# Performance work log

Hardware: AMD Instinct MI355X
Metric: run time of the kernel (lower is better)

## Reference

```python
import jax, jax.numpy as jnp
import numpy as np

B, N, D, M, H = 16, 196, 512, 20, 8


def setup_inputs() -> dict:
    key = jax.random.key(0)
    ks = jax.random.split(key, 8)
    s = 0.02  # small init scale for stable activations
    return {
        "F_clean": jax.random.normal(ks[0], (B, N, D), dtype=jnp.float32),
        "in_proj_w": jax.random.normal(ks[1], (3 * D, D), dtype=jnp.float32) * s,
        "in_proj_b": jnp.zeros((3 * D,), jnp.float32),
        "out_w": jax.random.normal(ks[2], (D, D), dtype=jnp.float32) * s,
        "out_b": jnp.zeros((D,), jnp.float32),
        "w1": jax.random.normal(ks[3], (D, D), dtype=jnp.float32) * s,
        "b1": jnp.zeros((D,), jnp.float32),
        "ln_g": jnp.ones((D,), jnp.float32),
        "ln_b": jnp.zeros((D,), jnp.float32),
        "w2": jax.random.normal(ks[4], (M, D), dtype=jnp.float32) * s,
        "b2": jnp.zeros((M,), jnp.float32),
        "templates": jax.random.normal(ks[5], (M, D), dtype=jnp.float32),
        "k": 51,  # int(D * sparsity_ratio=0.1)
    }


def reference(F_clean, in_proj_w, in_proj_b, out_w, out_b, w1, b1, ln_g, ln_b, w2, b2, templates, k):
    b, n, d = F_clean.shape
    hd = d // H
    # --- MultiheadAttention (batch_first, dropout inactive at eval) ---
    qkv = F_clean @ in_proj_w.T + in_proj_b  # [B,N,3D]
    q, kk, v = jnp.split(qkv, 3, axis=-1)
    to_heads = lambda x: x.reshape(b, n, H, hd).transpose(0, 2, 1, 3)  # [B,H,N,hd]
    q, kk, v = to_heads(q), to_heads(kk), to_heads(v)
    attn = jax.nn.softmax(jnp.einsum('bhqd,bhkd->bhqk', q, kk) / jnp.sqrt(jnp.float32(hd)), axis=-1)
    o = jnp.einsum('bhqk,bhkd->bhqd', attn, v).transpose(0, 2, 1, 3).reshape(b, n, d)
    F_enh = o @ out_w.T + out_b + F_clean  # residual
    # --- decompose MLP: Linear -> LayerNorm -> GELU(exact) -> Linear ---
    h = F_enh @ w1.T + b1
    mu = h.mean(-1, keepdims=True)
    var = h.var(-1, keepdims=True)
    h = (h - mu) / jnp.sqrt(var + 1e-5) * ln_g + ln_b
    h = jax.nn.gelu(h, approximate=False)
    Qp = h @ w2.T + b2  # [B,N,M]
    # --- outer-product expansion: [B,N,D,M] ---
    Q = F_clean[:, :, :, None] * templates.T[None, None] * Qp[:, :, None, :]
    # --- per-(b,n,m) abs-topk over D, scatter 0/1 mask, L2-normalize over D ---
    A = Q.transpose(0, 1, 3, 2)  # [B,N,M,D]
    _, idx = jax.lax.top_k(jnp.abs(A), k)
    mask = jnp.put_along_axis(jnp.zeros(A.shape, A.dtype), idx, 1.0, axis=-1, inplace=False)
    Qs = A * mask
    nrm = jnp.sqrt(jnp.sum(Qs * Qs, axis=-1, keepdims=True))
    Qn = Qs / jnp.maximum(nrm, 1e-6)  # torch F.normalize clamps norm to eps
    return Qn.transpose(0, 1, 3, 2)  # [B,N,D,M]
```

## Files before the change

kernel.cpp:

```cpp
#include <hip/hip_runtime.h>
#include <cmath>


typedef __attribute__((ext_vector_type(8))) short bf16x8v;
typedef __attribute__((ext_vector_type(4))) float f32x4v;

__device__ __forceinline__ unsigned short f2bf_rne(float x) {
  unsigned u = __float_as_uint(x);
  u += 0x7fffu + ((u >> 16) & 1u);
  return (unsigned short)(u >> 16);
}
__device__ __forceinline__ float bf2f(unsigned short h) {
  return __uint_as_float(((unsigned)h) << 16);
}
__device__ __forceinline__ void split3_1(float x,
    unsigned short& s0, unsigned short& s1, unsigned short& s2) {
  s0 = f2bf_rne(x); float r1 = x - bf2f(s0);
  s1 = f2bf_rne(r1); float r2 = r1 - bf2f(s1);
  s2 = f2bf_rne(r2);
}
__device__ __forceinline__ void split3_8(const float* xs,
    bf16x8v& o0, bf16x8v& o1, bf16x8v& o2) {
#pragma unroll
  for (int e = 0; e < 8; e++) {
    unsigned short a, b, c;
    split3_1(xs[e], a, b, c);
    o0[e] = (short)a; o1[e] = (short)b; o2[e] = (short)c;
  }
}

__global__ __launch_bounds__(256) void split4_kernel(
    const float* __restrict__ X0, unsigned short* __restrict__ O0, int n0,
    const float* __restrict__ X1, unsigned short* __restrict__ O1, int n1,
    const float* __restrict__ X2, unsigned short* __restrict__ O2, int n2,
    const float* __restrict__ X3, unsigned short* __restrict__ O3, int n3)
{
  int nb0 = n0 >> 11, nb1 = n1 >> 11, nb2 = n2 >> 11;
  int b = blockIdx.x;
  const float* X; unsigned short* O; long long i8, n;
  if (b < nb0)                   { X = X0; O = O0; n = n0; i8 = (long long)b * 256 + threadIdx.x; }
  else if (b < nb0 + nb1)        { X = X1; O = O1; n = n1; i8 = (long long)(b - nb0) * 256 + threadIdx.x; }
  else if (b < nb0 + nb1 + nb2)  { X = X2; O = O2; n = n2; i8 = (long long)(b - nb0 - nb1) * 256 + threadIdx.x; }
  else                           { X = X3; O = O3; n = n3; i8 = (long long)(b - nb0 - nb1 - nb2) * 256 + threadIdx.x; }
  const float4 aa = *(const float4*)(X + i8 * 8);
  const float4 bb = *(const float4*)(X + i8 * 8 + 4);
  float xs[8] = {aa.x, aa.y, aa.z, aa.w, bb.x, bb.y, bb.z, bb.w};
  bf16x8v o0, o1, o2;
  split3_8(xs, o0, o1, o2);
  *(bf16x8v*)(O + i8 * 8)          = o0;
  *(bf16x8v*)(O + n + i8 * 8)      = o1;
  *(bf16x8v*)(O + 2 * n + i8 * 8)  = o2;
}

#define GBK 32
#define AROWB 80
#define SPLIT_SZ (128 * AROWB)
#define BBASE (3 * SPLIT_SZ)

__global__ __launch_bounds__(256) void gemm_ps3_kernel(
    const unsigned short* __restrict__ As, const unsigned short* __restrict__ Bs,
    float* __restrict__ C, const float* __restrict__ bias,
    const float* __restrict__ res,
    int M, int N, int ldc, long long aPlane, long long bPlane,
    unsigned short* __restrict__ Cl, long long clPlane)
{
  __shared__ __align__(16) unsigned char smem[2 * BBASE];

  int tid = threadIdx.x;
  int lane = tid & 63, w = tid >> 6;
  int wrow = w >> 1, wcol = w & 1;
  int i0 = blockIdx.x * 128, j0 = blockIdx.y * 128;

  int r = tid >> 1, hh = tid & 1;
  int arow = i0 + r; if (arow > M - 1) arow = M - 1;
  int brow = j0 + r; if (brow > N - 1) brow = N - 1;
  const unsigned short* ap = As + (size_t)arow * 512 + hh * 16;
  const unsigned short* bp = Bs + (size_t)brow * 512 + hh * 16;
  unsigned swoff = (unsigned)r * AROWB + (unsigned)hh * 32;

  f32x4v acc[4][4];
#pragma unroll
  for (int fi = 0; fi < 4; fi++)
#pragma unroll
    for (int fj = 0; fj < 4; fj++) acc[fi][fj] = (f32x4v){0.f, 0.f, 0.f, 0.f};

  unsigned fr_a = (unsigned)(wrow * 64 + (lane & 15)) * AROWB + (unsigned)(lane >> 4) * 16;
  unsigned fr_b = (unsigned)(wcol * 64 + (lane & 15)) * AROWB + (unsigned)(lane >> 4) * 16 + BBASE;

  for (int k0 = 0; k0 < 512; k0 += GBK) {
    bf16x8v a0[3], a1[3], b0v[3], b1v[3];
#pragma unroll
    for (int s = 0; s < 3; s++) {
      a0[s]  = *(const bf16x8v*)(ap + s * aPlane + k0);
      a1[s]  = *(const bf16x8v*)(ap + s * aPlane + k0 + 8);
      b0v[s] = *(const bf16x8v*)(bp + s * bPlane + k0);
      b1v[s] = *(const bf16x8v*)(bp + s * bPlane + k0 + 8);
    }
    __syncthreads();
#pragma unroll
    for (int s = 0; s < 3; s++) {
      *(bf16x8v*)(smem + s * SPLIT_SZ + swoff)              = a0[s];
      *(bf16x8v*)(smem + s * SPLIT_SZ + swoff + 16)         = a1[s];
      *(bf16x8v*)(smem + BBASE + s * SPLIT_SZ + swoff)      = b0v[s];
      *(bf16x8v*)(smem + BBASE + s * SPLIT_SZ + swoff + 16) = b1v[s];
    }
    __syncthreads();

    bf16x8v af[4][3];
#pragma unroll
    for (int fi = 0; fi < 4; fi++)
#pragma unroll
      for (int s = 0; s < 3; s++)
        af[fi][s] = *(const bf16x8v*)(smem + s * SPLIT_SZ + fr_a + fi * (16 * AROWB));

#pragma unroll
    for (int fj = 0; fj < 4; fj++) {
      bf16x8v b0 = *(const bf16x8v*)(smem + 0 * SPLIT_SZ + fr_b + fj * (16 * AROWB));
      bf16x8v b1 = *(const bf16x8v*)(smem + 1 * SPLIT_SZ + fr_b + fj * (16 * AROWB));
      bf16x8v b2 = *(const bf16x8v*)(smem + 2 * SPLIT_SZ + fr_b + fj * (16 * AROWB));
#pragma unroll
      for (int fi = 0; fi < 4; fi++) {
        f32x4v c = acc[fi][fj];
        c = __builtin_amdgcn_mfma_f32_16x16x32_bf16(af[fi][2], b0, c, 0, 0, 0);
        c = __builtin_amdgcn_mfma_f32_16x16x32_bf16(af[fi][1], b1, c, 0, 0, 0);
        c = __builtin_amdgcn_mfma_f32_16x16x32_bf16(af[fi][0], b2, c, 0, 0, 0);
        c = __builtin_amdgcn_mfma_f32_16x16x32_bf16(af[fi][1], b0, c, 0, 0, 0);
        c = __builtin_amdgcn_mfma_f32_16x16x32_bf16(af[fi][0], b1, c, 0, 0, 0);
        c = __builtin_amdgcn_mfma_f32_16x16x32_bf16(af[fi][0], b0, c, 0, 0, 0);
        acc[fi][fj] = c;
      }
    }
  }

#pragma unroll
  for (int fi = 0; fi < 4; fi++) {
    int row0 = i0 + wrow * 64 + fi * 16 + (lane >> 4) * 4;
#pragma unroll
    for (int fj = 0; fj < 4; fj++) {
      int col = j0 + wcol * 64 + fj * 16 + (lane & 15);
      if (col >= N) continue;
      float badd = bias ? bias[col] : 0.0f;
      f32x4v v = acc[fi][fj];
#pragma unroll
      for (int rr = 0; rr < 4; rr++) {
        int row = row0 + rr;
        if (row < M) {
          float o = v[rr] + badd;
          if (res) o += res[(size_t)row * ldc + col];
          size_t idx = (size_t)row * ldc + col;
          if (Cl) {
            unsigned short l0, l1, l2;
            split3_1(o, l0, l1, l2);
            Cl[idx] = l0; Cl[idx + clPlane] = l1; Cl[idx + 2 * clPlane] = l2;
          } else {
            C[idx] = o;
          }
        }
      }
    }
  }
}

__global__ __launch_bounds__(256) void gemm_bf16x3_kernel(
    const float* __restrict__ A, const float* __restrict__ B,
    float* __restrict__ C, const float* __restrict__ bias,
    const float* __restrict__ res,
    int M, int N, int K, int lda, int ldb, int ldc,
    int zInner, long long aOuter, long long aInner,
    long long bOuter, long long bInner,
    long long cOuter, long long cInner,
    unsigned short* __restrict__ Cl, long long clPlane)
{
  int z = blockIdx.z;
  int zo = z / zInner, zi = z % zInner;
  A += zo * aOuter + zi * aInner;
  B += zo * bOuter + zi * bInner;
  long long coff = zo * cOuter + zi * cInner;
  if (C) C += coff;
  if (Cl) Cl += coff;

  __shared__ __align__(16) unsigned char smem[2 * BBASE];

  int tid = threadIdx.x;
  int lane = tid & 63, w = tid >> 6;
  int wrow = w >> 1, wcol = w & 1;
  int i0 = blockIdx.x * 128, j0 = blockIdx.y * 128;

  int srow = tid >> 1;
  int skh  = tid & 1;
  int arow = i0 + srow; if (arow > M - 1) arow = M - 1;
  int brow = j0 + srow; if (brow > N - 1) brow = N - 1;
  const float* aptr = A + (size_t)arow * lda + skh * 16;
  const float* bptr = B + (size_t)brow * ldb + skh * 16;
  unsigned swoff = (unsigned)srow * AROWB + (unsigned)skh * 32;

  f32x4v acc[4][4];
#pragma unroll
  for (int fi = 0; fi < 4; fi++)
#pragma unroll
    for (int fj = 0; fj < 4; fj++) acc[fi][fj] = (f32x4v){0.f, 0.f, 0.f, 0.f};

  unsigned fr_a = (unsigned)(wrow * 64 + (lane & 15)) * AROWB + (unsigned)(lane >> 4) * 16;
  unsigned fr_b = (unsigned)(wcol * 64 + (lane & 15)) * AROWB + (unsigned)(lane >> 4) * 16 + BBASE;

  for (int k0 = 0; k0 < K; k0 += GBK) {
    float av[16], bv[16];
    {
      const float4 q0 = *(const float4*)(aptr + k0);
      const float4 q1 = *(const float4*)(aptr + k0 + 4);
      const float4 q2 = *(const float4*)(aptr + k0 + 8);
      const float4 q3 = *(const float4*)(aptr + k0 + 12);
      av[0]=q0.x; av[1]=q0.y; av[2]=q0.z; av[3]=q0.w;
      av[4]=q1.x; av[5]=q1.y; av[6]=q1.z; av[7]=q1.w;
      av[8]=q2.x; av[9]=q2.y; av[10]=q2.z; av[11]=q2.w;
      av[12]=q3.x; av[13]=q3.y; av[14]=q3.z; av[15]=q3.w;
      const float4 r0 = *(const float4*)(bptr + k0);
      const float4 r1 = *(const float4*)(bptr + k0 + 4);
      const float4 r2 = *(const float4*)(bptr + k0 + 8);
      const float4 r3 = *(const float4*)(bptr + k0 + 12);
      bv[0]=r0.x; bv[1]=r0.y; bv[2]=r0.z; bv[3]=r0.w;
      bv[4]=r1.x; bv[5]=r1.y; bv[6]=r1.z; bv[7]=r1.w;
      bv[8]=r2.x; bv[9]=r2.y; bv[10]=r2.z; bv[11]=r2.w;
      bv[12]=r3.x; bv[13]=r3.y; bv[14]=r3.z; bv[15]=r3.w;
    }
    unsigned short ha[3][16], hb[3][16];
#pragma unroll
    for (int e = 0; e < 16; e++) {
      split3_1(av[e], ha[0][e], ha[1][e], ha[2][e]);
      split3_1(bv[e], hb[0][e], hb[1][e], hb[2][e]);
    }
    __syncthreads();
#pragma unroll
    for (int s = 0; s < 3; s++) {
      bf16x8v v0, v1, w0, w1;
#pragma unroll
      for (int e = 0; e < 8; e++) {
        v0[e] = (short)ha[s][e]; v1[e] = (short)ha[s][8 + e];
        w0[e] = (short)hb[s][e]; w1[e] = (short)hb[s][8 + e];
      }
      *(bf16x8v*)(smem + s * SPLIT_SZ + swoff)              = v0;
      *(bf16x8v*)(smem + s * SPLIT_SZ + swoff + 16)         = v1;
      *(bf16x8v*)(smem + BBASE + s * SPLIT_SZ + swoff)      = w0;
      *(bf16x8v*)(smem + BBASE + s * SPLIT_SZ + swoff + 16) = w1;
    }
    __syncthreads();

    bf16x8v af[4][3];
#pragma unroll
    for (int fi = 0; fi < 4; fi++)
#pragma unroll
      for (int s = 0; s < 3; s++)
        af[fi][s] = *(const bf16x8v*)(smem + s * SPLIT_SZ + fr_a + fi * (16 * AROWB));

#pragma unroll
    for (int fj = 0; fj < 4; fj++) {
      bf16x8v b0 = *(const bf16x8v*)(smem + 0 * SPLIT_SZ + fr_b + fj * (16 * AROWB));
      bf16x8v b1 = *(const bf16x8v*)(smem + 1 * SPLIT_SZ + fr_b + fj * (16 * AROWB));
      bf16x8v b2 = *(const bf16x8v*)(smem + 2 * SPLIT_SZ + fr_b + fj * (16 * AROWB));
#pragma unroll
      for (int fi = 0; fi < 4; fi++) {
        f32x4v c = acc[fi][fj];
        c = __builtin_amdgcn_mfma_f32_16x16x32_bf16(af[fi][2], b0, c, 0, 0, 0);
        c = __builtin_amdgcn_mfma_f32_16x16x32_bf16(af[fi][1], b1, c, 0, 0, 0);
        c = __builtin_amdgcn_mfma_f32_16x16x32_bf16(af[fi][0], b2, c, 0, 0, 0);
        c = __builtin_amdgcn_mfma_f32_16x16x32_bf16(af[fi][1], b0, c, 0, 0, 0);
        c = __builtin_amdgcn_mfma_f32_16x16x32_bf16(af[fi][0], b1, c, 0, 0, 0);
        c = __builtin_amdgcn_mfma_f32_16x16x32_bf16(af[fi][0], b0, c, 0, 0, 0);
        acc[fi][fj] = c;
      }
    }
  }

#pragma unroll
  for (int fi = 0; fi < 4; fi++) {
    int row0 = i0 + wrow * 64 + fi * 16 + (lane >> 4) * 4;
#pragma unroll
    for (int fj = 0; fj < 4; fj++) {
      int col = j0 + wcol * 64 + fj * 16 + (lane & 15);
      if (col >= N) continue;
      float badd = bias ? bias[col] : 0.0f;
      f32x4v v = acc[fi][fj];
#pragma unroll
      for (int rr = 0; rr < 4; rr++) {
        int row = row0 + rr;
        if (row < M) {
          float o = v[rr] + badd;
          if (res) o += res[(size_t)row * ldc + col];
          size_t idx = (size_t)row * ldc + col;
          if (Cl) {
            unsigned short l0, l1, l2;
            split3_1(o, l0, l1, l2);
            Cl[idx] = l0; Cl[idx + clPlane] = l1; Cl[idx + 2 * clPlane] = l2;
          } else {
            C[idx] = o;
          }
        }
      }
    }
  }
}

__global__ __launch_bounds__(256) void vtrans_kernel(
    const float* __restrict__ qkv, float* __restrict__ Vt)
{
  __shared__ float lds[224 * 65];
  int z = blockIdx.x;
  int b = z >> 3, h = z & 7;
  int tid = threadIdx.x;
  const float* src = qkv + ((size_t)b * 196) * 1536 + 1024 + h * 64;
  for (int idx = tid; idx < 224 * 64; idx += 256) {
    int kk = idx >> 6, d = idx & 63;
    lds[kk * 65 + d] = (kk < 196) ? src[(size_t)kk * 1536 + d] : 0.0f;
  }
  __syncthreads();
  float* dst = Vt + (size_t)z * (64 * 224);
  for (int idx = tid; idx < 64 * 224; idx += 256) {
    int d = idx / 224, kk = idx - d * 224;
    dst[idx] = lds[kk * 65 + d];
  }
}

__global__ __launch_bounds__(256) void softmax_kernel(float* __restrict__ S)
{
  int row = blockIdx.x * 4 + (threadIdx.x >> 6);
  int lane = threadIdx.x & 63;
  float* sr = S + (size_t)row * 196;
  double v[4];
#pragma unroll
  for (int t = 0; t < 4; t++) {
    int j = lane + 64 * t;
    v[t] = (j < 196) ? (double)sr[j] * 0.125 : -1e300;
  }
  double mx = fmax(fmax(v[0], v[1]), fmax(v[2], v[3]));
#pragma unroll
  for (int off = 1; off < 64; off <<= 1) mx = fmax(mx, __shfl_xor(mx, off));
  double e[4]; double s = 0.0;
#pragma unroll
  for (int t = 0; t < 4; t++) {
    int j = lane + 64 * t;
    e[t] = (j < 196) ? exp(v[t] - mx) : 0.0;
    s += e[t];
  }
#pragma unroll
  for (int off = 1; off < 64; off <<= 1) s += __shfl_xor(s, off);
  double inv = 1.0 / s;
#pragma unroll
  for (int t = 0; t < 4; t++) {
    int j = lane + 64 * t;
    if (j < 196) sr[j] = (float)(e[t] * inv);
  }
}

__global__ __launch_bounds__(256) void lnw2_kernel(
    const float* __restrict__ H, const float* __restrict__ g,
    const float* __restrict__ bb, const float* __restrict__ W2,
    const float* __restrict__ B2, float* __restrict__ Qp)
{
  int row = blockIdx.x;
  const float* hr = H + (size_t)row * 512;
  int tid = threadIdx.x, lane = tid & 63, wv = tid >> 6;
  __shared__ double red[8];
  __shared__ float y[512];
  double x0 = (double)hr[tid], x1 = (double)hr[tid + 256];
  double s = x0 + x1;
#pragma unroll
  for (int off = 1; off < 64; off <<= 1) s += __shfl_xor(s, off);
  if (lane == 0) red[wv] = s;
  __syncthreads();
  double mu = (red[0] + red[1] + red[2] + red[3]) * (1.0 / 512.0);
  double d0 = x0 - mu, d1 = x1 - mu;
  double q = d0 * d0 + d1 * d1;
#pragma unroll
  for (int off = 1; off < 64; off <<= 1) q += __shfl_xor(q, off);
  if (lane == 0) red[4 + wv] = q;
  __syncthreads();
  double var = (red[4] + red[5] + red[6] + red[7]) * (1.0 / 512.0);
  double inv = 1.0 / sqrt(var + 1e-5);
  double y0 = d0 * inv * (double)g[tid]       + (double)bb[tid];
  double y1 = d1 * inv * (double)g[tid + 256] + (double)bb[tid + 256];
  const double ISQRT2 = 0.70710678118654752440;
  double z0 = 0.5 * y0 * (1.0 + erf(y0 * ISQRT2));
  double z1 = 0.5 * y1 * (1.0 + erf(y1 * ISQRT2));
  y[tid] = (float)z0;
  y[tid + 256] = (float)z1;
  __syncthreads();

#pragma unroll 1
  for (int t = 0; t < 5; t++) {
    int m = wv * 5 + t;
    const float* wr = W2 + (size_t)m * 512;
    double acc = 0.0;
#pragma unroll
    for (int sE = 0; sE < 8; sE++) {
      int j = lane + 64 * sE;
      acc += (double)y[j] * (double)wr[j];
    }
#pragma unroll
    for (int off = 1; off < 64; off <<= 1) acc += __shfl_xor(acc, off);
    if (lane == 0) Qp[(size_t)row * 20 + m] = (float)(acc + (double)B2[m]);
  }
}

__device__ __forceinline__ void topk_finish32(
    const unsigned* uh, const unsigned* ul, const float* apf,
    unsigned thrh, bool exact, float qp, int g,
    unsigned long long* __restrict__ masks, float* __restrict__ qif, int lane)
{
  const int KSEL = 51;
  bool sel[8];
  if (exact) {
#pragma unroll
    for (int s = 0; s < 8; s++) sel[s] = (uh[s] >= thrh);
  } else {
    int cg = 0;
#pragma unroll
    for (int s = 0; s < 8; s++) {
      sel[s] = (uh[s] > thrh);
      cg += (int)__popcll(__ballot(sel[s]));
    }
    int need = KSEL - cg;
    bool tk[8];
#pragma unroll
    for (int s = 0; s < 8; s++) tk[s] = false;
    while (need > 0) {
      unsigned long long bk = 0ULL;
#pragma unroll
      for (int s = 0; s < 8; s++) {
        if (uh[s] == thrh && !tk[s]) {
          unsigned long long key = (1ULL << 41)
                                 | ((unsigned long long)ul[s] << 9)
                                 | ((unsigned long long)(7 - s) << 6)
                                 | (unsigned long long)(63 - lane);
          bk = key > bk ? key : bk;
        }
      }
#pragma unroll
      for (int off = 1; off < 64; off <<= 1) {
        unsigned long long ob = __shfl_xor(bk, off);
        bk = ob > bk ? ob : bk;
      }
      if ((int)(63 - (bk & 63ULL)) == lane) {
        int wsI = 7 - (int)((bk >> 6) & 7ULL);
        sel[wsI] = true;
        tk[wsI] = true;
      }
      need--;
    }
  }

  float ss = 0.f;
  unsigned long long selb[8];
#pragma unroll
  for (int s = 0; s < 8; s++) {
    selb[s] = __ballot((int)sel[s]);
    if (sel[s]) ss += apf[s] * apf[s];
  }
#pragma unroll
  for (int off = 1; off < 64; off <<= 1) ss += __shfl_xor(ss, off);
  float nrm = fabsf(qp) * sqrtf(ss);
  float qid = qp / fmaxf(nrm, 1e-6f);
  if (lane == 0) {
    qif[g] = qid;
#pragma unroll
    for (int s = 0; s < 8; s++) masks[(size_t)g * 8 + s] = selb[s];
  }
}

__global__ __launch_bounds__(256) void topk_select_kernel(
    const float* __restrict__ F, const float* __restrict__ T,
    const float* __restrict__ Qp, unsigned long long* __restrict__ masks,
    float* __restrict__ qif)
{
  const int KSEL = 51;
  int wid = blockIdx.x * 4 + (threadIdx.x >> 6);
  int lane = threadIdx.x & 63;
  int g0 = wid * 2;
  int bn = g0 / 20, m0 = g0 - bn * 20;
  const float* Frow = F + (size_t)bn * 512;
  const float* T0r = T + (size_t)m0 * 512;
  const float* T1r = T0r + 512;

  unsigned uh0[8], ul0[8], uh1[8], ul1[8];
  float ap0[8], ap1[8];
#pragma unroll
  for (int s = 0; s < 8; s++) {
    double fd = (double)Frow[lane + 64 * s];
    double p0 = fd * (double)T0r[lane + 64 * s];
    double p1 = fd * (double)T1r[lane + 64 * s];
    unsigned long long u0 =
        (unsigned long long)__double_as_longlong(p0) & 0x7fffffffffffffffULL;
    unsigned long long u1 =
        (unsigned long long)__double_as_longlong(p1) & 0x7fffffffffffffffULL;
    uh0[s] = (unsigned)(u0 >> 32); ul0[s] = (unsigned)u0;
    uh1[s] = (unsigned)(u1 >> 32); ul1[s] = (unsigned)u1;
    ap0[s] = (float)fabs(p0); ap1[s] = (float)fabs(p1);
  }

  unsigned mx0 = 0u, mn0 = 0xffffffffu, mx1 = 0u, mn1 = 0xffffffffu;
#pragma unroll
  for (int s = 0; s < 8; s++) {
    mx0 = uh0[s] > mx0 ? uh0[s] : mx0;  mn0 = uh0[s] < mn0 ? uh0[s] : mn0;
    mx1 = uh1[s] > mx1 ? uh1[s] : mx1;  mn1 = uh1[s] < mn1 ? uh1[s] : mn1;
  }
#pragma unroll
  for (int off = 1; off < 64; off <<= 1) {
    unsigned a = __shfl_xor(mx0, off); mx0 = a > mx0 ? a : mx0;
    unsigned b = __shfl_xor(mn0, off); mn0 = b < mn0 ? b : mn0;
    unsigned c = __shfl_xor(mx1, off); mx1 = c > mx1 ? c : mx1;
    unsigned d = __shfl_xor(mn1, off); mn1 = d < mn1 ? d : mn1;
  }

  unsigned lo0 = mn0, hi0 = mx0 + 1u, lo1 = mn1, hi1 = mx1 + 1u;
  bool ex0 = false, ex1 = false;
  bool dn0 = (hi0 - lo0 <= 1u), dn1 = (hi1 - lo1 <= 1u);
  while (!(dn0 && dn1)) {
    if (!dn0) {
      unsigned mid = lo0 + ((hi0 - lo0) >> 1);
      int c = 0;
#pragma unroll
      for (int s = 0; s < 8; s++) c += (int)__popcll(__ballot(uh0[s] >= mid));
      if (c >= KSEL) { lo0 = mid; if (c == KSEL) { ex0 = true; dn0 = true; } }
      else hi0 = mid;
      dn0 = dn0 || (hi0 - lo0 <= 1u);
    }
    if (!dn1) {
      unsigned mid = lo1 + ((hi1 - lo1) >> 1);
      int c = 0;
#pragma unroll
      for (int s = 0; s < 8; s++) c += (int)__popcll(__ballot(uh1[s] >= mid));
      if (c >= KSEL) { lo1 = mid; if (c == KSEL) { ex1 = true; dn1 = true; } }
      else hi1 = mid;
      dn1 = dn1 || (hi1 - lo1 <= 1u);
    }
  }
  topk_finish32(uh0, ul0, ap0, lo0, ex0, Qp[g0],     g0,     masks, qif, lane);
  topk_finish32(uh1, ul1, ap1, lo1, ex1, Qp[g0 + 1], g0 + 1, masks, qif, lane);
}

__global__ __launch_bounds__(256) void topk_write_kernel(
    const float* __restrict__ F, const float* __restrict__ T,
    const unsigned long long* __restrict__ masks,
    const float* __restrict__ qif, float* __restrict__ out)
{
  int bn = blockIdx.x;
  int tid = threadIdx.x;
  __shared__ unsigned long long mw[20][8];
  __shared__ float qf[20];
  __shared__ float vt[256][21];
  if (tid < 160) ((unsigned long long*)mw)[tid] = masks[(size_t)bn * 160 + tid];
  if (tid < 20) qf[tid] = qif[(size_t)bn * 20 + tid];
  const float* Frow = F + (size_t)bn * 512;
  float* orow = out + (size_t)bn * 10240;
  __syncthreads();

#pragma unroll
  for (int half = 0; half < 2; half++) {
    int d = half * 256 + tid;
    float fd = Frow[d];
    int dw = d >> 6, db = d & 63;
#pragma unroll
    for (int m = 0; m < 20; m++) {
      bool sel = (mw[m][dw] >> db) & 1ULL;
      float tv = T[(size_t)m * 512 + d];
      vt[tid][m] = sel ? fd * tv * qf[m] : 0.0f;
    }
    __syncthreads();
#pragma unroll
    for (int k = 0; k < 5; k++) {
      int flat = (k * 256 + tid) * 4;
      float v[4];
#pragma unroll
      for (int e = 0; e < 4; e++) {
        int fe = flat + e;
        int dl = fe / 20;
        int mm = fe - dl * 20;
        v[e] = vt[dl][mm];
      }
      float4 o = {v[0], v[1], v[2], v[3]};
      *(float4*)&orow[half * 5120 + flat] = o;
    }
    __syncthreads();
  }
}

extern "C" void kernel_launch(void* const* d_in, const int* in_sizes, int n_in,
                              void* d_out, int out_size, void* d_ws, size_t ws_size,
                              hipStream_t stream) {
  const float* F    = (const float*)d_in[0];
  const float* Wqkv = (const float*)d_in[1];
  const float* bqkv = (const float*)d_in[2];
  const float* Wo   = (const float*)d_in[3];
  const float* bo   = (const float*)d_in[4];
  const float* W1   = (const float*)d_in[5];
  const float* b1   = (const float*)d_in[6];
  const float* lng  = (const float*)d_in[7];
  const float* lnb  = (const float*)d_in[8];
  const float* W2   = (const float*)d_in[9];
  const float* b2   = (const float*)d_in[10];
  const float* Tm   = (const float*)d_in[11];
  float* out = (float*)d_out;

  float* ws     = (float*)d_ws;
  float* qkv    = ws;
  float* scores = ws + 4816896;
  float* Vt     = ws + 9734144;
  float* h1     = ws + 11569152;
  float* Qp     = ws + 13174784;
  unsigned short* Wos   = (unsigned short*)(ws + 13237504);
  unsigned short* W1s   = (unsigned short*)(ws + 13630720);
  unsigned short* Omgs  = (unsigned short*)(ws + 14023936);
  unsigned short* Fenhs = (unsigned short*)(ws + 16432384);
  unsigned short* Fs    = (unsigned short*)scores;
  unsigned short* Wqkvs = (unsigned short*)(scores + 2408448);
  unsigned long long* masks = (unsigned long long*)qkv;
  float* qifb = (float*)(masks + (size_t)62720 * 8);
  dim3 blk(256);

  split4_kernel<<<dim3(1424), blk, 0, stream>>>(
      F, Fs, 1605632, Wqkv, Wqkvs, 786432,
      Wo, Wos, 262144, W1, W1s, 262144);

  gemm_ps3_kernel<<<dim3(25, 12), blk, 0, stream>>>(
      Fs, Wqkvs, qkv, bqkv, nullptr, 3136, 1536, 1536, 1605632LL, 786432LL,
      nullptr, 0);

  vtrans_kernel<<<dim3(128), blk, 0, stream>>>(qkv, Vt);

  gemm_bf16x3_kernel<<<dim3(2, 2, 128), blk, 0, stream>>>(
      qkv, qkv + 512, scores, nullptr, nullptr,
      196, 196, 64, 1536, 1536, 196,
      8, 196LL * 1536, 64, 196LL * 1536, 64, 8LL * 38416, 38416,
      nullptr, 0);

  softmax_kernel<<<dim3(6272), blk, 0, stream>>>(scores);

  gemm_bf16x3_kernel<<<dim3(2, 1, 128), blk, 0, stream>>>(
      scores, Vt, nullptr, nullptr, nullptr,
      196, 64, 196, 196, 224, 512,
      8, 8LL * 38416, 38416, 8LL * 14336, 14336, 100352, 64,
      Omgs, 1605632LL);

  gemm_ps3_kernel<<<dim3(25, 4), blk, 0, stream>>>(
      Omgs, Wos, nullptr, bo, F, 3136, 512, 512, 1605632LL, 262144LL,
      Fenhs, 1605632LL);

  gemm_ps3_kernel<<<dim3(25, 4), blk, 0, stream>>>(
      Fenhs, W1s, h1, b1, nullptr, 3136, 512, 512, 1605632LL, 262144LL,
      nullptr, 0);

  lnw2_kernel<<<dim3(3136), blk, 0, stream>>>(h1, lng, lnb, W2, b2, Qp);

  topk_select_kernel<<<dim3(7840), blk, 0, stream>>>(F, Tm, Qp, masks, qifb);

  topk_write_kernel<<<dim3(3136), blk, 0, stream>>>(F, Tm, masks, qifb, out);
}
```

Before: 370.1 us.

## Fold out-projection into W1 and fuse F·W1 into QKV GEMM

```diff
diff --git a/kernel.cpp b/kernel.cpp
--- a/kernel.cpp
+++ b/kernel.cpp
@@ -19,37 +19,140 @@
   s1 = f2bf_rne(r1); float r2 = r1 - bf2f(s1);
   s2 = f2bf_rne(r2);
 }
-__device__ __forceinline__ void split3_8(const float* xs,
-    bf16x8v& o0, bf16x8v& o1, bf16x8v& o2) {
+
+__global__ __launch_bounds__(256) void prep_kernel(
+    const float* __restrict__ F, unsigned short* __restrict__ Fs,
+    const float* __restrict__ Wqkv, const float* __restrict__ W1,
+    unsigned short* __restrict__ Walls,
+    const float* __restrict__ Wo, unsigned short* __restrict__ Wcs,
+    float* __restrict__ Vt,
+    const float* __restrict__ bo, const float* __restrict__ b1,
+    float* __restrict__ bcomb,
+    const float* __restrict__ bqkv, float* __restrict__ biasAll)
+{
+  int b = blockIdx.x;
+  int tid = threadIdx.x;
+
+  if (b < 1296) {
+    const float* X; unsigned short* O; long long i8, pstride;
+    if (b < 784)       { X = F;    O = Fs;              pstride = 1605632; i8 = (long long)b * 256 + tid; }
+    else if (b < 1168) { X = Wqkv; O = Walls;           pstride = 1048576; i8 = (long long)(b - 784) * 256 + tid; }
+    else               { X = W1;   O = Walls + 786432;  pstride = 1048576; i8 = (long long)(b - 1168) * 256 + tid; }
+    const float4 aa = *(const float4*)(X + i8 * 8);
+    const float4 bb = *(const float4*)(X + i8 * 8 + 4);
+    float xs[8] = {aa.x, aa.y, aa.z, aa.w, bb.x, bb.y, bb.z, bb.w};
+    bf16x8v o0, o1, o2;
+#pragma unroll
+    for (int e = 0; e < 8; e++) {
+      unsigned short s0, s1, s2;
+      split3_1(xs[e], s0, s1, s2);
+      o0[e] = (short)s0; o1[e] = (short)s1; o2[e] = (short)s2;
+    }
+    *(bf16x8v*)(O + i8 * 8)               = o0;
+    *(bf16x8v*)(O + pstride + i8 * 8)     = o1;
+    *(bf16x8v*)(O + 2 * pstride + i8 * 8) = o2;
+    return;
+  }
+
+  if (b < 1360) {
+    __shared__ __align__(16) float As[16][68];
+    __shared__ __align__(16) float Bs[16][68];
+    int local = b - 1296;
+    int i0 = (local >> 3) * 64, j0 = (local & 7) * 64;
+    int tx = tid & 15, ty = tid >> 4;
+    double acc[4][4];
+#pragma unroll
+    for (int i = 0; i < 4; i++)
+#pragma unroll
+      for (int j = 0; j < 4; j++) acc[i][j] = 0.0;
+    for (int k0 = 0; k0 < 512; k0 += 16) {
+#pragma unroll
+      for (int rr = 0; rr < 4; rr++) {
+        int r = ty + 16 * rr;
+        As[tx][r] = W1[(size_t)(i0 + r) * 512 + k0 + tx];
+      }
+      {
+        int j = tid & 63, c0 = (tid >> 6) * 4;
+#pragma unroll
+        for (int cc = 0; cc < 4; cc++) {
+          int c = c0 + cc;
+          Bs[c][j] = Wo[(size_t)(k0 + c) * 512 + j0 + j];
+        }
+      }
+      __syncthreads();
+      float cf[4][4];
+#pragma unroll
+      for (int i = 0; i < 4; i++)
+#pragma unroll
+        for (int j = 0; j < 4; j++) cf[i][j] = 0.0f;
+#pragma unroll
+      for (int kk = 0; kk < 16; kk++) {
+        float4 a4 = *(const float4*)&As[kk][ty * 4];
+        float4 b4 = *(const float4*)&Bs[kk][tx * 4];
+        float av[4] = {a4.x, a4.y, a4.z, a4.w};
+        float bv[4] = {b4.x, b4.y, b4.z, b4.w};
+#pragma unroll
+        for (int i = 0; i < 4; i++)
+#pragma unroll
+          for (int j = 0; j < 4; j++) cf[i][j] = fmaf(av[i], bv[j], cf[i][j]);
+      }
+#pragma unroll
+      for (int i = 0; i < 4; i++)
+#pragma unroll
+        for (int j = 0; j < 4; j++) acc[i][j] += (double)cf[i][j];
+      __syncthreads();
+    }
+#pragma unroll
+    for (int i = 0; i < 4; i++) {
+      int gi = i0 + ty * 4 + i;
+#pragma unroll
+      for (int j = 0; j < 4; j++) {
+        int gj = j0 + tx * 4 + j;
+        float o = (float)acc[i][j];
+        unsigned short l0, l1, l2;
+        split3_1(o, l0, l1, l2);
+        size_t idx = (size_t)gi * 512 + gj;
+        Wcs[idx] = l0; Wcs[idx + 262144] = l1; Wcs[idx + 524288] = l2;
+      }
+    }
+    return;
+  }
+
+  if (b < 1472) {
+    long long p0 = (long long)(b - 1360) * 2048 + tid * 8;
+#pragma unroll
+    for (int e = 0; e < 8; e++) {
+      long long pf = p0 + e;
+      int z = (int)(pf / 1792);
+      int r = (int)(pf - (long long)z * 1792);
+      int d = r / 28, kk = r - d * 28;
+      Vt[(size_t)z * 14336 + (size_t)d * 224 + 196 + kk] = 0.0f;
+    }
+    return;
+  }
+
+  if (b == 1472) {
+#pragma unroll
+    for (int half = 0; half < 2; half++) {
+      int n = tid + half * 256;
+      const float* wr = W1 + (size_t)n * 512;
+      double acc = 0.0;
+      for (int k = 0; k < 512; k += 4) {
+        float4 wv = *(const float4*)&wr[k];
+        float4 bv = *(const float4*)&bo[k];
+        acc += (double)wv.x * bv.x + (double)wv.y * bv.y +
+               (double)wv.z * bv.z + (double)wv.w * bv.w;
+      }
+      bcomb[n] = (float)(acc + (double)b1[n]);
+    }
+    return;
+  }
+
 #pragma unroll
   for (int e = 0; e < 8; e++) {
-    unsigned short a, b, c;
-    split3_1(xs[e], a, b, c);
-    o0[e] = (short)a; o1[e] = (short)b; o2[e] = (short)c;
-  }
-}
-
-__global__ __launch_bounds__(256) void split4_kernel(
-    const float* __restrict__ X0, unsigned short* __restrict__ O0, int n0,
-    const float* __restrict__ X1, unsigned short* __restrict__ O1, int n1,
-    const float* __restrict__ X2, unsigned short* __restrict__ O2, int n2,
-    const float* __restrict__ X3, unsigned short* __restrict__ O3, int n3)
-{
-  int nb0 = n0 >> 11, nb1 = n1 >> 11, nb2 = n2 >> 11;
-  int b = blockIdx.x;
-  const float* X; unsigned short* O; long long i8, n;
-  if (b < nb0)                   { X = X0; O = O0; n = n0; i8 = (long long)b * 256 + threadIdx.x; }
-  else if (b < nb0 + nb1)        { X = X1; O = O1; n = n1; i8 = (long long)(b - nb0) * 256 + threadIdx.x; }
-  else if (b < nb0 + nb1 + nb2)  { X = X2; O = O2; n = n2; i8 = (long long)(b - nb0 - nb1) * 256 + threadIdx.x; }
-  else                           { X = X3; O = O3; n = n3; i8 = (long long)(b - nb0 - nb1 - nb2) * 256 + threadIdx.x; }
-  const float4 aa = *(const float4*)(X + i8 * 8);
-  const float4 bb = *(const float4*)(X + i8 * 8 + 4);
-  float xs[8] = {aa.x, aa.y, aa.z, aa.w, bb.x, bb.y, bb.z, bb.w};
-  bf16x8v o0, o1, o2;
-  split3_8(xs, o0, o1, o2);
-  *(bf16x8v*)(O + i8 * 8)          = o0;
-  *(bf16x8v*)(O + n + i8 * 8)      = o1;
-  *(bf16x8v*)(O + 2 * n + i8 * 8)  = o2;
+    int idx = tid * 8 + e;
+    biasAll[idx] = (idx < 1536) ? bqkv[idx] : 0.0f;
+  }
 }
 
 #define GBK 32
@@ -61,10 +164,16 @@
     const unsigned short* __restrict__ As, const unsigned short* __restrict__ Bs,
     float* __restrict__ C, const float* __restrict__ bias,
     const float* __restrict__ res,
-    int M, int N, int ldc, long long aPlane, long long bPlane,
-    unsigned short* __restrict__ Cl, long long clPlane)
+    int M, int N, int ldc, int ldres,
+    long long aPlane, long long bPlane,
+    int kLen, long long cZStride,
+    float* __restrict__ VtOut)
 {
   __shared__ __align__(16) unsigned char smem[2 * BBASE];
+
+  int z = blockIdx.z;
+  int kOff = z * kLen;
+  C += (size_t)z * cZStride;
 
   int tid = threadIdx.x;
   int lane = tid & 63, w = tid >> 6;
@@ -74,8 +183,8 @@
   int r = tid >> 1, hh = tid & 1;
   int arow = i0 + r; if (arow > M - 1) arow = M - 1;
   int brow = j0 + r; if (brow > N - 1) brow = N - 1;
-  const unsigned short* ap = As + (size_t)arow * 512 + hh * 16;
-  const unsigned short* bp = Bs + (size_t)brow * 512 + hh * 16;
+  const unsigned short* ap = As + (size_t)arow * 512 + hh * 16 + kOff;
+  const unsigned short* bp = Bs + (size_t)brow * 512 + hh * 16 + kOff;
   unsigned swoff = (unsigned)r * AROWB + (unsigned)hh * 32;
 
   f32x4v acc[4][4];
@@ -87,7 +196,7 @@
   unsigned fr_a = (unsigned)(wrow * 64 + (lane & 15)) * AROWB + (unsigned)(lane >> 4) * 16;
   unsigned fr_b = (unsigned)(wcol * 64 + (lane & 15)) * AROWB + (unsigned)(lane >> 4) * 16 + BBASE;
 
-  for (int k0 = 0; k0 < 512; k0 += GBK) {
+  for (int k0 = 0; k0 < kLen; k0 += GBK) {
     bf16x8v a0[3], a1[3], b0v[3], b1v[3];
 #pragma unroll
     for (int s = 0; s < 3; s++) {
@@ -139,21 +248,22 @@
     for (int fj = 0; fj < 4; fj++) {
       int col = j0 + wcol * 64 + fj * 16 + (lane & 15);
       if (col >= N) continue;
-      float badd = bias ? bias[col] : 0.0f;
+      float badd = (bias && z == 0) ? bias[col] : 0.0f;
       f32x4v v = acc[fi][fj];
 #pragma unroll
       for (int rr = 0; rr < 4; rr++) {
         int row = row0 + rr;
         if (row < M) {
           float o = v[rr] + badd;
-          if (res) o += res[(size_t)row * ldc + col];
-          size_t idx = (size_t)row * ldc + col;
-          if (Cl) {
-            unsigned short l0, l1, l2;
-            split3_1(o, l0, l1, l2);
-            Cl[idx] = l0; Cl[idx + clPlane] = l1; Cl[idx + 2 * clPlane] = l2;
+          if (res && z == 0) o += res[(size_t)row * ldres + col];
+          if (VtOut && col >= 1024 && col < 1536) {
+            int d = col - 1024;
+            int bb = row / 196;
+            int kk = row - bb * 196;
+            int zz = bb * 8 + (d >> 6);
+            VtOut[(size_t)zz * 14336 + (size_t)(d & 63) * 224 + kk] = o;
           } else {
-            C[idx] = o;
+            C[(size_t)row * ldc + col] = o;
           }
         }
       }
@@ -300,26 +410,6 @@
   }
 }
 
-__global__ __launch_bounds__(256) void vtrans_kernel(
-    const float* __restrict__ qkv, float* __restrict__ Vt)
-{
-  __shared__ float lds[224 * 65];
-  int z = blockIdx.x;
-  int b = z >> 3, h = z & 7;
-  int tid = threadIdx.x;
-  const float* src = qkv + ((size_t)b * 196) * 1536 + 1024 + h * 64;
-  for (int idx = tid; idx < 224 * 64; idx += 256) {
-    int kk = idx >> 6, d = idx & 63;
-    lds[kk * 65 + d] = (kk < 196) ? src[(size_t)kk * 1536 + d] : 0.0f;
-  }
-  __syncthreads();
-  float* dst = Vt + (size_t)z * (64 * 224);
-  for (int idx = tid; idx < 64 * 224; idx += 256) {
-    int d = idx / 224, kk = idx - d * 224;
-    dst[idx] = lds[kk * 65 + d];
-  }
-}
-
 __global__ __launch_bounds__(256) void softmax_kernel(float* __restrict__ S)
 {
   int row = blockIdx.x * 4 + (threadIdx.x >> 6);
@@ -361,7 +451,10 @@
   int tid = threadIdx.x, lane = tid & 63, wv = tid >> 6;
   __shared__ double red[8];
   __shared__ float y[512];
-  double x0 = (double)hr[tid], x1 = (double)hr[tid + 256];
+  double x0 = (double)hr[tid]       + (double)hr[tid + 1605632]
+            + (double)hr[tid + 3211264] + (double)hr[tid + 4816896];
+  double x1 = (double)hr[tid + 256] + (double)hr[tid + 256 + 1605632]
+            + (double)hr[tid + 256 + 3211264] + (double)hr[tid + 256 + 4816896];
   double s = x0 + x1;
 #pragma unroll
   for (int off = 1; off < 64; off <<= 1) s += __shfl_xor(s, off);
@@ -600,36 +693,33 @@
   const float* Tm   = (const float*)d_in[11];
   float* out = (float*)d_out;
 
-  float* ws     = (float*)d_ws;
-  float* qkv    = ws;
-  float* scores = ws + 4816896;
-  float* Vt     = ws + 9734144;
-  float* h1     = ws + 11569152;
-  float* Qp     = ws + 13174784;
-  unsigned short* Wos   = (unsigned short*)(ws + 13237504);
-  unsigned short* W1s   = (unsigned short*)(ws + 13630720);
-  unsigned short* Omgs  = (unsigned short*)(ws + 14023936);
-  unsigned short* Fenhs = (unsigned short*)(ws + 16432384);
-  unsigned short* Fs    = (unsigned short*)scores;
-  unsigned short* Wqkvs = (unsigned short*)(scores + 2408448);
-  unsigned long long* masks = (unsigned long long*)qkv;
-  float* qifb = (float*)(masks + (size_t)62720 * 8);
+  float* ws = (float*)d_ws;
+  float* qkvw   = ws;
+  float* scores = ws + 6422528;
+  float* Vt     = ws + 11339776;
+  float* h1p    = ws + 13174784;
+  float* Qp     = ws + 19597312;
+  float* bcomb  = ws + 19660032;
+  float* biasAll= ws + 19660544;
+  unsigned long long* masks = (unsigned long long*)(ws + 19662592);
+  float* qifb   = ws + 20666112;
+  unsigned short* Fs    = (unsigned short*)(ws + 20728832);
+  unsigned short* Walls = (unsigned short*)(ws + 23137280);
+  unsigned short* Wcs   = (unsigned short*)(ws + 24710144);
+  unsigned short* Omgs  = (unsigned short*)(ws + 25103360);
   dim3 blk(256);
 
-  split4_kernel<<<dim3(1424), blk, 0, stream>>>(
-      F, Fs, 1605632, Wqkv, Wqkvs, 786432,
-      Wo, Wos, 262144, W1, W1s, 262144);
-
-  gemm_ps3_kernel<<<dim3(25, 12), blk, 0, stream>>>(
-      Fs, Wqkvs, qkv, bqkv, nullptr, 3136, 1536, 1536, 1605632LL, 786432LL,
-      nullptr, 0);
-
-  vtrans_kernel<<<dim3(128), blk, 0, stream>>>(qkv, Vt);
+  prep_kernel<<<dim3(1474), blk, 0, stream>>>(
+      F, Fs, Wqkv, W1, Walls, Wo, Wcs, Vt, bo, b1, bcomb, bqkv, biasAll);
+
+  gemm_ps3_kernel<<<dim3(25, 16, 1), blk, 0, stream>>>(
+      Fs, Walls, qkvw, biasAll, nullptr,
+      3136, 2048, 2048, 0, 1605632LL, 1048576LL, 512, 0LL, Vt);
 
   gemm_bf16x3_kernel<<<dim3(2, 2, 128), blk, 0, stream>>>(
-      qkv, qkv + 512, scores, nullptr, nullptr,
-      196, 196, 64, 1536, 1536, 196,
-      8, 196LL * 1536, 64, 196LL * 1536, 64, 8LL * 38416, 38416,
+      qkvw, qkvw + 512, scores, nullptr, nullptr,
+      196, 196, 64, 2048, 2048, 196,
+      8, 196LL * 2048, 64, 196LL * 2048, 64, 8LL * 38416, 38416,
       nullptr, 0);
 
   softmax_kernel<<<dim3(6272), blk, 0, stream>>>(scores);
@@ -640,15 +730,11 @@
       8, 8LL * 38416, 38416, 8LL * 14336, 14336, 100352, 64,
       Omgs, 1605632LL);
 
-  gemm_ps3_kernel<<<dim3(25, 4), blk, 0, stream>>>(
-      Omgs, Wos, nullptr, bo, F, 3136, 512, 512, 1605632LL, 262144LL,
-      Fenhs, 1605632LL);
-
-  gemm_ps3_kernel<<<dim3(25, 4), blk, 0, stream>>>(
-      Fenhs, W1s, h1, b1, nullptr, 3136, 512, 512, 1605632LL, 262144LL,
-      nullptr, 0);
-
-  lnw2_kernel<<<dim3(3136), blk, 0, stream>>>(h1, lng, lnb, W2, b2, Qp);
+  gemm_ps3_kernel<<<dim3(25, 4, 4), blk, 0, stream>>>(
+      Omgs, Wcs, h1p, bcomb, qkvw + 1536,
+      3136, 512, 512, 2048, 1605632LL, 262144LL, 128, 1605632LL, nullptr);
+
+  lnw2_kernel<<<dim3(3136), blk, 0, stream>>>(h1p, lng, lnb, W2, b2, Qp);
 
   topk_select_kernel<<<dim3(7840), blk, 0, stream>>>(F, Tm, Qp, masks, qifb);
 
```

New measurement: 316.0 us. 1.17x faster.
